# Performance work log

Hardware: AMD Instinct MI355X
Metric: run time of the kernel (lower is better)

## Reference

```python
import jax, jax.numpy as jnp
import numpy as np
import math

N_LAYERS = 8
D = 1024
H = 16
DK = D // H
T = 1024
V = 32000
B = 2
DFF = 4 * D
EPS = 1e-5


def layernorm(x, scale, bias):
    mu = jnp.mean(x, axis=-1, keepdims=True)
    var = jnp.mean(jnp.square(x - mu), axis=-1, keepdims=True)
    return (x - mu) * jax.lax.rsqrt(var + EPS) * scale + bias


def setup_inputs() -> dict:
    key = jax.random.key(0)
    ks = jax.random.split(key, 32)
    s = 0.02
    rn = lambda k, shape: jax.random.normal(k, shape, dtype=jnp.float32) * s
    x = jax.random.randint(ks[0], (B, T), 0, V)
    return {
        "x": x,
        "inp_emb": rn(ks[1], (V, D)),
        "pos_emb": rn(ks[2], (T, D)),
        # per-layer weights stacked on leading layer axis; per-head wq/wk/wv are
        # concatenated along the output dim (mathematically identical to the
        # per-head nn.Linear list in the torch code)
        "wq": rn(ks[3], (N_LAYERS, D, D)), "bq": jnp.zeros((N_LAYERS, D), jnp.float32),
        "wk": rn(ks[4], (N_LAYERS, D, D)), "bk": jnp.zeros((N_LAYERS, D), jnp.float32),
        "wv": rn(ks[5], (N_LAYERS, D, D)), "bv": jnp.zeros((N_LAYERS, D), jnp.float32),
        "wo": rn(ks[6], (N_LAYERS, D, D)), "bo": jnp.zeros((N_LAYERS, D), jnp.float32),
        "w1": rn(ks[7], (N_LAYERS, D, DFF)), "b1": jnp.zeros((N_LAYERS, DFF), jnp.float32),
        "w2": rn(ks[8], (N_LAYERS, DFF, D)), "b2": jnp.zeros((N_LAYERS, D), jnp.float32),
        "ln1_s": jnp.ones((N_LAYERS, D), jnp.float32), "ln1_b": jnp.zeros((N_LAYERS, D), jnp.float32),
        "ln2_s": jnp.ones((N_LAYERS, D), jnp.float32), "ln2_b": jnp.zeros((N_LAYERS, D), jnp.float32),
        "lno_s": jnp.ones((D,), jnp.float32), "lno_b": jnp.zeros((D,), jnp.float32),
        "w_out": rn(ks[9], (D, V)),
    }


def reference(x, inp_emb, pos_emb, wq, bq, wk, bk, wv, bv, wo, bo,
              w1, b1, w2, b2, ln1_s, ln1_b, ln2_s, ln2_b, lno_s, lno_b, w_out):
    h = inp_emb[x] + pos_emb[jnp.arange(T)]            # [B,T,D]
    causal = jnp.tril(jnp.ones((T, T), dtype=bool))    # [T,T]
    scale = 1.0 / math.sqrt(DK)
    for i in range(N_LAYERS):
        # --- multi-head causal attention ---
        xn = layernorm(h, ln1_s[i], ln1_b[i])
        q = (xn @ wq[i] + bq[i]).reshape(B, T, H, DK)
        k = (xn @ wk[i] + bk[i]).reshape(B, T, H, DK)
        v = (xn @ wv[i] + bv[i]).reshape(B, T, H, DK)
        scores = jnp.einsum('bqhd,bkhd->bhqk', q, k) * scale
        scores = jnp.where(causal, scores, -jnp.inf)
        att = jax.nn.softmax(scores, axis=-1)           # [B,H,T,T]
        y = jnp.einsum('bhqk,bkhd->bqhd', att, v).reshape(B, T, D)
        h = h + y @ wo[i] + bo[i]
        # --- feed-forward ---
        xn = layernorm(h, ln2_s[i], ln2_b[i])
        h = h + jax.nn.gelu(xn @ w1[i] + b1[i], approximate=False) @ w2[i] + b2[i]
    h = layernorm(h, lno_s, lno_b)
    return h @ w_out                                    # logits [B,T,V]
```

## Files before the change

### kernel.cpp

```cpp
#include <hip/hip_runtime.h>
#include <cmath>

#define D_MODEL 1024
#define N_HEADS 16
#define DKH     64
#define SEQ_T   1024
#define BATCH   2
#define VOCAB   32000
#define DFF_    4096
#define NLAYERS 8

typedef __bf16 bf16x8 __attribute__((ext_vector_type(8)));
typedef __bf16 bf16x4v __attribute__((ext_vector_type(4)));
typedef float  f32x4  __attribute__((ext_vector_type(4)));

__device__ __forceinline__ float gelu_f(float x) {
    return 0.5f * x * (1.0f + erff(x * 0.70710678118654752f));
}

__device__ __forceinline__ void gload_lds16(const void* g, void* l) {
    __builtin_amdgcn_global_load_lds(
        (const __attribute__((address_space(1))) void*)g,
        (__attribute__((address_space(3))) void*)l, 16, 0, 0);
}

__global__ __launch_bounds__(256) void embed_kernel(
    const int* __restrict__ x, const float* __restrict__ inp_emb,
    const float* __restrict__ pos_emb, float* __restrict__ h)
{
    const int idx = blockIdx.x * 256 + threadIdx.x;
    const int bt  = idx >> 10;
    const int d   = idx & 1023;
    const int t   = bt & (SEQ_T - 1);
    const int tok = x[bt];
    h[idx] = inp_emb[(size_t)tok * D_MODEL + d] + pos_emb[(size_t)t * D_MODEL + d];
}

__device__ __forceinline__ void ln_row(
    const float* __restrict__ x, const float* __restrict__ sc,
    const float* __restrict__ bi, __bf16* __restrict__ o, int row, int tid)
{
    const int c = tid * 4;
    const float4 v = *(const float4*)(x + (size_t)row * D_MODEL + c);
    float sum = v.x + v.y + v.z + v.w;
    float sq  = v.x * v.x + v.y * v.y + v.z * v.z + v.w * v.w;
    #pragma unroll
    for (int off = 32; off > 0; off >>= 1) {
        sum += __shfl_xor(sum, off);
        sq  += __shfl_xor(sq, off);
    }
    __shared__ float ssum[4], ssq[4];
    const int wave = tid >> 6, lane = tid & 63;
    if (lane == 0) { ssum[wave] = sum; ssq[wave] = sq; }
    __syncthreads();
    sum = ssum[0] + ssum[1] + ssum[2] + ssum[3];
    sq  = ssq[0]  + ssq[1]  + ssq[2]  + ssq[3];
    const float mu  = sum * (1.0f / D_MODEL);
    const float var = sq * (1.0f / D_MODEL) - mu * mu;
    const float rs  = rsqrtf(var + 1e-5f);
    const float4 s4 = *(const float4*)(sc + c);
    const float4 b4 = *(const float4*)(bi + c);
    bf16x4v ov;
    ov[0] = (__bf16)((v.x - mu) * rs * s4.x + b4.x);
    ov[1] = (__bf16)((v.y - mu) * rs * s4.y + b4.y);
    ov[2] = (__bf16)((v.z - mu) * rs * s4.z + b4.z);
    ov[3] = (__bf16)((v.w - mu) * rs * s4.w + b4.w);
    *(bf16x4v*)(o + (size_t)row * D_MODEL + c) = ov;
}

__global__ __launch_bounds__(256) void layernorm_kernel(
    const float* __restrict__ x, const float* __restrict__ sc,
    const float* __restrict__ bi, __bf16* __restrict__ o)
{
    ln_row(x, sc, bi, o, blockIdx.x, threadIdx.x);
}

__global__ __launch_bounds__(256) void prep_ln_kernel(
    const float* __restrict__ h, const float* __restrict__ ln_s,
    const float* __restrict__ ln_b, __bf16* __restrict__ xn,
    const float* __restrict__ wq, const float* __restrict__ wk,
    const float* __restrict__ wv, const float* __restrict__ wo,
    const float* __restrict__ w1, const float* __restrict__ w2,
    const float* __restrict__ bq, const float* __restrict__ bk,
    const float* __restrict__ bv,
    __bf16* __restrict__ wqkvT, __bf16* __restrict__ woT,
    __bf16* __restrict__ w1T, __bf16* __restrict__ w2T,
    float* __restrict__ bqkv,
    const float* __restrict__ wout, __bf16* __restrict__ woutT)
{
    const int tid = threadIdx.x;
    const int b   = blockIdx.x;

    if (b < 2048) {
        ln_row(h, ln_s, ln_b, xn, b, tid);
        return;
    }
    const int pb = b - 2048;
    if (pb >= 12288 && pb < 12300) {
        const int j = (pb - 12288) * 256 + tid;
        bqkv[j] = (j < 1024) ? bq[j] : (j < 2048 ? bk[j - 1024] : bv[j - 2048]);
        return;
    }

    __shared__ __bf16 tile[32][36];
    const float* in;
    __bf16* out;
    int K, N, kb0, nb0;
    if (pb < 4096) {
        const int w = pb >> 10, t = pb & 1023;
        K = 1024; N = 1024; kb0 = (t >> 5) * 32; nb0 = (t & 31) * 32;
        in  = (w == 0) ? wq : (w == 1) ? wk : (w == 2) ? wv : wo;
        out = (w == 3) ? woT : wqkvT + (size_t)w * 1024 * 1024;
    } else if (pb < 8192) {
        const int t = pb - 4096;
        K = 1024; N = 4096; kb0 = (t >> 7) * 32; nb0 = (t & 127) * 32;
        in = w1; out = w1T;
    } else if (pb < 12288) {
        const int t = pb - 8192;
        K = 4096; N = 1024; kb0 = (t >> 5) * 32; nb0 = (t & 31) * 32;
        in = w2; out = w2T;
    } else {
        const int t = pb - 12300;
        K = 1024; N = VOCAB; kb0 = (t & 31) * 32; nb0 = (t >> 5) * 32;
        in = wout; out = woutT;
    }

    {
        const int rr = tid >> 3, c4 = (tid & 7) * 4;
        const float4 v = *(const float4*)(in + (size_t)(kb0 + rr) * N + nb0 + c4);
        tile[rr][c4 + 0] = (__bf16)v.x;
        tile[rr][c4 + 1] = (__bf16)v.y;
        tile[rr][c4 + 2] = (__bf16)v.z;
        tile[rr][c4 + 3] = (__bf16)v.w;
    }
    __syncthreads();
    {
        const int cc = tid >> 3, r4 = (tid & 7) * 4;
        bf16x4v ov;
        ov[0] = tile[r4 + 0][cc];
        ov[1] = tile[r4 + 1][cc];
        ov[2] = tile[r4 + 2][cc];
        ov[3] = tile[r4 + 3][cc];
        *(bf16x4v*)(out + (size_t)(nb0 + cc) * K + kb0 + r4) = ov;
    }
}

template <int BN_T, int EPI, typename OutT, bool NT = false>
__global__ __launch_bounds__(256) void gemm_bt(
    const __bf16* __restrict__ A, const __bf16* __restrict__ Bt,
    const float* __restrict__ bias, const float* __restrict__ res,
    OutT* __restrict__ C, int M, int N, int K)
{
    constexpr int NF  = BN_T / 32;
    constexpr int NCB = BN_T / 8;
    __shared__ __align__(16) char smem[(128 + BN_T) * 64 * 2];
    __bf16* As = (__bf16*)smem;
    __bf16* Bs = As + 128 * 64;

    const int tid  = threadIdx.x;
    const int wave = tid >> 6;
    const int lane = tid & 63;
    const int r    = lane & 15;
    const int kb   = lane >> 4;
    const int wm   = wave >> 1;
    const int wn   = wave & 1;

    const int ntm = gridDim.x;
    const int nwg = ntm * gridDim.y;
    int bid = blockIdx.y * ntm + blockIdx.x;
    if ((nwg & 7) == 0) bid = (bid & 7) * (nwg >> 3) + (bid >> 3);
    const int bm = (bid % ntm) * 128;
    const int bn = (bid / ntm) * BN_T;

    const int srow = lane >> 3;
    const int sg   = lane & 7;

    f32x4 acc[4][NF] = {};

    for (int k0 = 0; k0 < K; k0 += 64) {
        #pragma unroll
        for (int i = 0; i < 4; ++i) {
            const int c    = i * 4 + wave;
            const int row  = c * 8 + srow;
            const int scol = (sg ^ (row & 7)) * 8;
            gload_lds16(A + (size_t)(bm + row) * K + k0 + scol, &As[c * 512]);
        }
        #pragma unroll
        for (int i = 0; i < NCB / 4; ++i) {
            const int c    = i * 4 + wave;
            const int row  = c * 8 + srow;
            const int scol = (sg ^ (row & 7)) * 8;
            gload_lds16(Bt + (size_t)(bn + row) * K + k0 + scol, &Bs[c * 512]);
        }
        __syncthreads();

        #pragma unroll
        for (int s = 0; s < 2; ++s) {
            bf16x8 af[4];
            #pragma unroll
            for (int m = 0; m < 4; ++m) {
                const int row = wm * 64 + m * 16 + r;
                const int g   = (s * 4 + kb) ^ (row & 7);
                af[m] = *(const bf16x8*)&As[row * 64 + g * 8];
            }
            #pragma unroll
            for (int n = 0; n < NF; ++n) {
                const int row = wn * (NF * 16) + n * 16 + r;
                const int g   = (s * 4 + kb) ^ (row & 7);
                const bf16x8 bfr = *(const bf16x8*)&Bs[row * 64 + g * 8];
                #pragma unroll
                for (int m = 0; m < 4; ++m)
                    acc[m][n] = __builtin_amdgcn_mfma_f32_16x16x32_bf16(af[m], bfr, acc[m][n], 0, 0, 0);
            }
        }
        __syncthreads();
    }

    if constexpr (NT) {
        float* Cs = (float*)smem;
        #pragma unroll
        for (int cchunk = 0; cchunk < 4; ++cchunk) {
            if (wm == (cchunk >> 1)) {
                #pragma unroll
                for (int mm = 0; mm < 2; ++mm) {
                    const int m = (cchunk & 1) * 2 + mm;
                    #pragma unroll
                    for (int n = 0; n < NF; ++n) {
                        const int col = wn * (NF * 16) + n * 16 + r;
                        const float bv = bias ? bias[bn + col] : 0.0f;
                        #pragma unroll
                        for (int rg = 0; rg < 4; ++rg)
                            Cs[(mm * 16 + kb * 4 + rg) * 132 + col] = acc[m][n][rg] + bv;
                    }
                }
            }
            __syncthreads();
            const int rrow = tid >> 3, g8 = tid & 7;
            const size_t grow = (size_t)(bm + cchunk * 32 + rrow) * N + bn;
            #pragma unroll
            for (int j = 0; j < 4; ++j) {
                const f32x4 v = *(const f32x4*)&Cs[rrow * 132 + j * 32 + g8 * 4];
                __builtin_nontemporal_store(v, (f32x4*)((float*)C + grow + j * 32 + g8 * 4));
            }
            __syncthreads();
        }
        return;
    }

    #pragma unroll
    for (int m = 0; m < 4; ++m) {
        const int row = bm + wm * 64 + m * 16 + kb * 4;
        #pragma unroll
        for (int n = 0; n < NF; ++n) {
            const int col = bn + wn * (NF * 16) + n * 16 + r;
            const float bv = bias ? bias[col] : 0.0f;
            #pragma unroll
            for (int rg = 0; rg < 4; ++rg) {
                float v = acc[m][n][rg] + bv;
                if constexpr (EPI == 1) v += res[(size_t)(row + rg) * N + col];
                if constexpr (EPI == 2) v = gelu_f(v);
                C[(size_t)(row + rg) * N + col] = (OutT)v;
            }
        }
    }
}

struct AttnState {
    float m[4];
    float l[4];
    f32x4 yacc[4];
};

template <bool MASK>
__device__ __forceinline__ void attn_tile_step(
    AttnState& st, const bf16x8 (&qf)[2], int q0, int kt,
    int wave, int r, int kb,
    const __bf16 (*K_lds)[72], const __bf16 (*V_lds)[72],
    __bf16 (*P_row)[72])
{
    f32x4 sacc[4] = {};
    #pragma unroll
    for (int kc = 0; kc < 2; ++kc) {
        #pragma unroll
        for (int g = 0; g < 4; ++g) {
            const bf16x8 kf = *(const bf16x8*)&K_lds[g * 16 + r][kc * 32 + kb * 8];
            sacc[g] = __builtin_amdgcn_mfma_f32_16x16x32_bf16(qf[kc], kf, sacc[g], 0, 0, 0);
        }
    }

    float s[4][4], p[4][4];
    #pragma unroll
    for (int g = 0; g < 4; ++g) {
        #pragma unroll
        for (int rg = 0; rg < 4; ++rg) {
            if constexpr (MASK) {
                const int key = kt * 64 + g * 16 + r;
                const int qq  = q0 + wave * 16 + kb * 4 + rg;
                s[g][rg] = (key <= qq) ? sacc[g][rg] * 0.125f : -INFINITY;
            } else {
                s[g][rg] = sacc[g][rg] * 0.125f;
            }
        }
    }

    float mt[4];
    #pragma unroll
    for (int rg = 0; rg < 4; ++rg)
        mt[rg] = fmaxf(fmaxf(s[0][rg], s[1][rg]), fmaxf(s[2][rg], s[3][rg]));
    #pragma unroll
    for (int off = 1; off < 16; off <<= 1) {
        #pragma unroll
        for (int rg = 0; rg < 4; ++rg) mt[rg] = fmaxf(mt[rg], __shfl_xor(mt[rg], off));
    }

    bool grow = false;
    #pragma unroll
    for (int rg = 0; rg < 4; ++rg) grow |= (mt[rg] > st.m[rg] + 8.0f);
    if (__any(grow)) {
        #pragma unroll
        for (int rg = 0; rg < 4; ++rg) {
            const float mn   = fmaxf(st.m[rg], mt[rg]);
            const float corr = __expf(st.m[rg] - mn);
            st.l[rg] *= corr;
            st.m[rg]  = mn;
            #pragma unroll
            for (int n = 0; n < 4; ++n) st.yacc[n][rg] *= corr;
        }
    }

    float psum[4];
    #pragma unroll
    for (int rg = 0; rg < 4; ++rg) {
        psum[rg] = 0.0f;
        #pragma unroll
        for (int g = 0; g < 4; ++g) {
            p[g][rg] = __expf(s[g][rg] - st.m[rg]);
            psum[rg] += p[g][rg];
        }
    }
    #pragma unroll
    for (int off = 1; off < 16; off <<= 1) {
        #pragma unroll
        for (int rg = 0; rg < 4; ++rg) psum[rg] += __shfl_xor(psum[rg], off);
    }
    #pragma unroll
    for (int rg = 0; rg < 4; ++rg) st.l[rg] += psum[rg];

    #pragma unroll
    for (int g = 0; g < 4; ++g) {
        #pragma unroll
        for (int rg = 0; rg < 4; ++rg)
            P_row[kb * 4 + rg][g * 16 + r] = (__bf16)p[g][rg];
    }
    const bf16x8 pa0 = *(const bf16x8*)&P_row[r][kb * 8];
    const bf16x8 pa1 = *(const bf16x8*)&P_row[r][32 + kb * 8];

    #pragma unroll
    for (int n = 0; n < 4; ++n) {
        const int vrow = n * 16 + r;
        const int swz  = (vrow >> 3) & 7;
        const bf16x8 vf0 = *(const bf16x8*)&V_lds[vrow][(kb ^ swz) * 8];
        st.yacc[n] = __builtin_amdgcn_mfma_f32_16x16x32_bf16(pa0, vf0, st.yacc[n], 0, 0, 0);
    }
    #pragma unroll
    for (int n = 0; n < 4; ++n) {
        const int vrow = n * 16 + r;
        const int swz  = (vrow >> 3) & 7;
        const bf16x8 vf1 = *(const bf16x8*)&V_lds[vrow][((kb + 4) ^ swz) * 8];
        st.yacc[n] = __builtin_amdgcn_mfma_f32_16x16x32_bf16(pa1, vf1, st.yacc[n], 0, 0, 0);
    }
}

__global__ __launch_bounds__(256) void attn_mfma_kernel(
    const __bf16* __restrict__ qkv, __bf16* __restrict__ y)
{
    constexpr int QS = 3 * D_MODEL;
    __shared__ __align__(16) __bf16 K_lds[64][72];
    __shared__ __align__(16) __bf16 V_lds[64][72];
    __shared__ __align__(16) __bf16 P_lds[4][16][72];

    const int tid  = threadIdx.x;
    const int wave = tid >> 6;
    const int lane = tid & 63;
    const int r    = lane & 15;
    const int kb   = lane >> 4;

    const int ip  = blockIdx.x;
    const int q0A = ip * 64;
    const int q0B = (15 - ip) * 64;
    const int b   = blockIdx.y >> 4;
    const int h   = blockIdx.y & 15;

    const __bf16* qp = qkv + (size_t)b * SEQ_T * QS + h * DKH;
    const __bf16* kp = qp + D_MODEL;
    const __bf16* vp = qp + 2 * D_MODEL;
    __bf16* yp = y + (size_t)b * SEQ_T * D_MODEL + h * DKH;

    bf16x8 qfA[2], qfB[2];
    {
        const int qrA = q0A + wave * 16 + r;
        const int qrB = q0B + wave * 16 + r;
        #pragma unroll
        for (int kc = 0; kc < 2; ++kc) {
            qfA[kc] = *(const bf16x8*)(qp + (size_t)qrA * QS + kc * 32 + kb * 8);
            qfB[kc] = *(const bf16x8*)(qp + (size_t)qrB * QS + kc * 32 + kb * 8);
        }
    }

    AttnState stA, stB;
    #pragma unroll
    for (int rg = 0; rg < 4; ++rg) {
        stA.m[rg] = -INFINITY; stA.l[rg] = 0.0f;
        stB.m[rg] = -INFINITY; stB.l[rg] = 0.0f;
    }
    #pragma unroll
    for (int n = 0; n < 4; ++n) { stA.yacc[n] = {}; stB.yacc[n] = {}; }

    const int skey = tid >> 2;
    const int sg16 = (tid & 3) * 16;
    const int swz0 = ((sg16 >> 3) & 7) * 8;
    const int swz1 = (((sg16 + 8) >> 3) & 7) * 8;

    const int ntiles = 16 - ip;

    bf16x8 kr0, kr1, vr0, vr1;
    {
        const size_t go = (size_t)skey * QS;
        kr0 = *(const bf16x8*)(kp + go + sg16);
        kr1 = *(const bf16x8*)(kp + go + sg16 + 8);
        vr0 = *(const bf16x8*)(vp + go + sg16);
        vr1 = *(const bf16x8*)(vp + go + sg16 + 8);
    }

    for (int kt = 0; kt < ntiles; ++kt) {
        *(bf16x8*)&K_lds[skey][sg16]     = kr0;
        *(bf16x8*)&K_lds[skey][sg16 + 8] = kr1;
        #pragma unroll
        for (int j = 0; j < 8; ++j)
            V_lds[sg16 + j][skey ^ swz0] = vr0[j];
        #pragma unroll
        for (int j = 0; j < 8; ++j)
            V_lds[sg16 + 8 + j][skey ^ swz1] = vr1[j];
        __syncthreads();

        if (kt + 1 < ntiles) {
            const size_t go = (size_t)((kt + 1) * 64 + skey) * QS;
            kr0 = *(const bf16x8*)(kp + go + sg16);
            kr1 = *(const bf16x8*)(kp + go + sg16 + 8);
            vr0 = *(const bf16x8*)(vp + go + sg16);
            vr1 = *(const bf16x8*)(vp + go + sg16 + 8);
        }

        if (kt == ntiles - 1)
            attn_tile_step<true >(stB, qfB, q0B, kt, wave, r, kb, K_lds, V_lds, P_lds[wave]);
        else
            attn_tile_step<false>(stB, qfB, q0B, kt, wave, r, kb, K_lds, V_lds, P_lds[wave]);
        if (kt <= ip) {
            if (kt == ip)
                attn_tile_step<true >(stA, qfA, q0A, kt, wave, r, kb, K_lds, V_lds, P_lds[wave]);
            else
                attn_tile_step<false>(stA, qfA, q0A, kt, wave, r, kb, K_lds, V_lds, P_lds[wave]);
        }
        __syncthreads();
    }

    float invA[4], invB[4];
    #pragma unroll
    for (int rg = 0; rg < 4; ++rg) {
        invA[rg] = 1.0f / stA.l[rg];
        invB[rg] = 1.0f / stB.l[rg];
    }
    #pragma unroll
    for (int n = 0; n < 4; ++n) {
        #pragma unroll
        for (int rg = 0; rg < 4; ++rg) {
            const int rowA = q0A + wave * 16 + kb * 4 + rg;
            const int rowB = q0B + wave * 16 + kb * 4 + rg;
            yp[(size_t)rowA * D_MODEL + n * 16 + r] = (__bf16)(stA.yacc[n][rg] * invA[rg]);
            yp[(size_t)rowB * D_MODEL + n * 16 + r] = (__bf16)(stB.yacc[n][rg] * invB[rg]);
        }
    }
}

extern "C" void kernel_launch(void* const* d_in, const int* in_sizes, int n_in,
                              void* d_out, int out_size, void* d_ws, size_t ws_size,
                              hipStream_t stream)
{
    const int*   x       = (const int*)  d_in[0];
    const float* inp_emb = (const float*)d_in[1];
    const float* pos_emb = (const float*)d_in[2];
    const float* wq = (const float*)d_in[3];
    const float* bq = (const float*)d_in[4];
    const float* wk = (const float*)d_in[5];
    const float* bk = (const float*)d_in[6];
    const float* wv = (const float*)d_in[7];
    const float* bv = (const float*)d_in[8];
    const float* wo = (const float*)d_in[9];
    const float* bo = (const float*)d_in[10];
    const float* w1 = (const float*)d_in[11];
    const float* b1 = (const float*)d_in[12];
    const float* w2 = (const float*)d_in[13];
    const float* b2 = (const float*)d_in[14];
    const float* ln1_s = (const float*)d_in[15];
    const float* ln1_b = (const float*)d_in[16];
    const float* ln2_s = (const float*)d_in[17];
    const float* ln2_b = (const float*)d_in[18];
    const float* lno_s = (const float*)d_in[19];
    const float* lno_b = (const float*)d_in[20];
    const float* w_out = (const float*)d_in[21];

    const int M = BATCH * SEQ_T;
    const size_t MB = 1u << 20;

    char* w = (char*)d_ws;
    float*  h     = (float*) (w + 0);
    __bf16* xn    = (__bf16*)(w + 8  * MB);
    __bf16* yb    = (__bf16*)(w + 12 * MB);
    __bf16* sh    = (__bf16*)(w + 16 * MB);
    __bf16* wqkvT = (__bf16*)(w + 32 * MB);
    __bf16* woT   = (__bf16*)(w + 38 * MB);
    __bf16* w1T   = (__bf16*)(w + 40 * MB);
    __bf16* w2T   = (__bf16*)(w + 48 * MB);
    float*  bqkv  = (float*) (w + 56 * MB);
    __bf16* woutT = (__bf16*)(w + 57 * MB);

    embed_kernel<<<dim3(M * D_MODEL / 256), 256, 0, stream>>>(x, inp_emb, pos_emb, h);

    for (int i = 0; i < NLAYERS; ++i) {
        const size_t wOff  = (size_t)i * D_MODEL * D_MODEL;
        const size_t w1Off = (size_t)i * D_MODEL * DFF_;

        const int nblk = 2048 + 12300 + (i == 0 ? 32000 : 0);
        prep_ln_kernel<<<dim3(nblk), 256, 0, stream>>>(
            h, ln1_s + i * D_MODEL, ln1_b + i * D_MODEL, xn,
            wq + wOff, wk + wOff, wv + wOff, wo + wOff, w1 + w1Off, w2 + w1Off,
            bq + i * D_MODEL, bk + i * D_MODEL, bv + i * D_MODEL,
            wqkvT, woT, w1T, w2T, bqkv,
            (i == 0) ? w_out : nullptr, woutT);

        gemm_bt<64, 0, __bf16><<<dim3(M / 128, 3 * D_MODEL / 64), 256, 0, stream>>>(
            xn, wqkvT, bqkv, nullptr, sh, M, 3 * D_MODEL, D_MODEL);
        attn_mfma_kernel<<<dim3(8, BATCH * N_HEADS), 256, 0, stream>>>(sh, yb);
        gemm_bt<64, 1, float><<<dim3(M / 128, D_MODEL / 64), 256, 0, stream>>>(
            yb, woT, bo + i * D_MODEL, h, h, M, D_MODEL, D_MODEL);
        layernorm_kernel<<<dim3(M), 256, 0, stream>>>(h, ln2_s + i * D_MODEL, ln2_b + i * D_MODEL, xn);
        gemm_bt<128, 2, __bf16><<<dim3(M / 128, DFF_ / 128), 256, 0, stream>>>(
            xn, w1T, b1 + i * DFF_, nullptr, sh, M, DFF_, D_MODEL);
        gemm_bt<64, 1, float><<<dim3(M / 128, D_MODEL / 64), 256, 0, stream>>>(
            sh, w2T, b2 + i * D_MODEL, h, h, M, D_MODEL, DFF_);
    }

    layernorm_kernel<<<dim3(M), 256, 0, stream>>>(h, lno_s, lno_b, xn);
    gemm_bt<128, 0, float, true><<<dim3(M / 128, VOCAB / 128), 256, 0, stream>>>(
        xn, woutT, nullptr, nullptr, (float*)d_out, M, VOCAB, D_MODEL);
}
```

Baseline: 1.661 ms.

## Widen weight transpose tiles to 32x64 and simplify nontemporal GEMM epilogue

The fused LN/weight-transpose kernel now handles 32x64 tiles per block, so each thread loads two float4s and writes a 16-byte bf16x8 vector. This halves the block count and makes the transposed stores wider. The GEMM drops its LDS-staged, coalesced nontemporal epilogue for the output projection and writes directly with per-element nontemporal stores, with shared memory split into separate A/B arrays. The epilogue change gives up coalesced 16-byte logits writes in favor of scattered scalar stores, which may hurt the large vocab GEMM.

Measured after the change: 1.697 ms. +2.2%, slower.

```diff
diff --git a/kernel.cpp b/kernel.cpp
--- a/kernel.cpp
+++ b/kernel.cpp
@@ -96,52 +96,56 @@
         return;
     }
     const int pb = b - 2048;
-    if (pb >= 12288 && pb < 12300) {
-        const int j = (pb - 12288) * 256 + tid;
+    if (pb >= 6144 && pb < 6156) {
+        const int j = (pb - 6144) * 256 + tid;
         bqkv[j] = (j < 1024) ? bq[j] : (j < 2048 ? bk[j - 1024] : bv[j - 2048]);
         return;
     }
 
-    __shared__ __bf16 tile[32][36];
+    __shared__ __bf16 tile[32][72];
     const float* in;
     __bf16* out;
     int K, N, kb0, nb0;
-    if (pb < 4096) {
-        const int w = pb >> 10, t = pb & 1023;
-        K = 1024; N = 1024; kb0 = (t >> 5) * 32; nb0 = (t & 31) * 32;
+    if (pb < 2048) {
+        const int w = pb >> 9, t = pb & 511;
+        K = 1024; N = 1024; kb0 = (t >> 4) * 32; nb0 = (t & 15) * 64;
         in  = (w == 0) ? wq : (w == 1) ? wk : (w == 2) ? wv : wo;
         out = (w == 3) ? woT : wqkvT + (size_t)w * 1024 * 1024;
-    } else if (pb < 8192) {
+    } else if (pb < 4096) {
+        const int t = pb - 2048;
+        K = 1024; N = 4096; kb0 = (t >> 6) * 32; nb0 = (t & 63) * 64;
+        in = w1; out = w1T;
+    } else if (pb < 6144) {
         const int t = pb - 4096;
-        K = 1024; N = 4096; kb0 = (t >> 7) * 32; nb0 = (t & 127) * 32;
-        in = w1; out = w1T;
-    } else if (pb < 12288) {
-        const int t = pb - 8192;
-        K = 4096; N = 1024; kb0 = (t >> 5) * 32; nb0 = (t & 31) * 32;
+        K = 4096; N = 1024; kb0 = (t >> 4) * 32; nb0 = (t & 15) * 64;
         in = w2; out = w2T;
     } else {
-        const int t = pb - 12300;
-        K = 1024; N = VOCAB; kb0 = (t & 31) * 32; nb0 = (t >> 5) * 32;
+        const int t = pb - 6156;
+        K = 1024; N = VOCAB; kb0 = (t & 31) * 32; nb0 = (t >> 5) * 64;
         in = wout; out = woutT;
     }
 
     {
-        const int rr = tid >> 3, c4 = (tid & 7) * 4;
-        const float4 v = *(const float4*)(in + (size_t)(kb0 + rr) * N + nb0 + c4);
-        tile[rr][c4 + 0] = (__bf16)v.x;
-        tile[rr][c4 + 1] = (__bf16)v.y;
-        tile[rr][c4 + 2] = (__bf16)v.z;
-        tile[rr][c4 + 3] = (__bf16)v.w;
+        const int rr = tid >> 3, c8 = (tid & 7) * 8;
+        const float* p = in + (size_t)(kb0 + rr) * N + nb0 + c8;
+        const float4 v0 = *(const float4*)p;
+        const float4 v1 = *(const float4*)(p + 4);
+        tile[rr][c8 + 0] = (__bf16)v0.x;
+        tile[rr][c8 + 1] = (__bf16)v0.y;
+        tile[rr][c8 + 2] = (__bf16)v0.z;
+        tile[rr][c8 + 3] = (__bf16)v0.w;
+        tile[rr][c8 + 4] = (__bf16)v1.x;
+        tile[rr][c8 + 5] = (__bf16)v1.y;
+        tile[rr][c8 + 6] = (__bf16)v1.z;
+        tile[rr][c8 + 7] = (__bf16)v1.w;
     }
     __syncthreads();
     {
-        const int cc = tid >> 3, r4 = (tid & 7) * 4;
-        bf16x4v ov;
-        ov[0] = tile[r4 + 0][cc];
-        ov[1] = tile[r4 + 1][cc];
-        ov[2] = tile[r4 + 2][cc];
-        ov[3] = tile[r4 + 3][cc];
-        *(bf16x4v*)(out + (size_t)(nb0 + cc) * K + kb0 + r4) = ov;
+        const int cc = tid >> 2, k8 = (tid & 3) * 8;
+        bf16x8 ov;
+        #pragma unroll
+        for (int e = 0; e < 8; ++e) ov[e] = tile[k8 + e][cc];
+        *(bf16x8*)(out + (size_t)(nb0 + cc) * K + kb0 + k8) = ov;
     }
 }
 
@@ -153,9 +157,8 @@
 {
     constexpr int NF  = BN_T / 32;
     constexpr int NCB = BN_T / 8;
-    __shared__ __align__(16) char smem[(128 + BN_T) * 64 * 2];
-    __bf16* As = (__bf16*)smem;
-    __bf16* Bs = As + 128 * 64;
+    __shared__ __bf16 As[128 * 64];
+    __shared__ __bf16 Bs[BN_T * 64];
 
     const int tid  = threadIdx.x;
     const int wave = tid >> 6;
@@ -216,37 +219,6 @@
         __syncthreads();
     }
 
-    if constexpr (NT) {
-        float* Cs = (float*)smem;
-        #pragma unroll
-        for (int cchunk = 0; cchunk < 4; ++cchunk) {
-            if (wm == (cchunk >> 1)) {
-                #pragma unroll
-                for (int mm = 0; mm < 2; ++mm) {
-                    const int m = (cchunk & 1) * 2 + mm;
-                    #pragma unroll
-                    for (int n = 0; n < NF; ++n) {
-                        const int col = wn * (NF * 16) + n * 16 + r;
-                        const float bv = bias ? bias[bn + col] : 0.0f;
-                        #pragma unroll
-                        for (int rg = 0; rg < 4; ++rg)
-                            Cs[(mm * 16 + kb * 4 + rg) * 132 + col] = acc[m][n][rg] + bv;
-                    }
-                }
-            }
-            __syncthreads();
-            const int rrow = tid >> 3, g8 = tid & 7;
-            const size_t grow = (size_t)(bm + cchunk * 32 + rrow) * N + bn;
-            #pragma unroll
-            for (int j = 0; j < 4; ++j) {
-                const f32x4 v = *(const f32x4*)&Cs[rrow * 132 + j * 32 + g8 * 4];
-                __builtin_nontemporal_store(v, (f32x4*)((float*)C + grow + j * 32 + g8 * 4));
-            }
-            __syncthreads();
-        }
-        return;
-    }
-
     #pragma unroll
     for (int m = 0; m < 4; ++m) {
         const int row = bm + wm * 64 + m * 16 + kb * 4;
@@ -259,7 +231,11 @@
                 float v = acc[m][n][rg] + bv;
                 if constexpr (EPI == 1) v += res[(size_t)(row + rg) * N + col];
                 if constexpr (EPI == 2) v = gelu_f(v);
-                C[(size_t)(row + rg) * N + col] = (OutT)v;
+                if constexpr (NT) {
+                    __builtin_nontemporal_store((OutT)v, &C[(size_t)(row + rg) * N + col]);
+                } else {
+                    C[(size_t)(row + rg) * N + col] = (OutT)v;
+                }
             }
         }
     }
@@ -530,7 +506,7 @@
         const size_t wOff  = (size_t)i * D_MODEL * D_MODEL;
         const size_t w1Off = (size_t)i * D_MODEL * DFF_;
 
-        const int nblk = 2048 + 12300 + (i == 0 ? 32000 : 0);
+        const int nblk = 2048 + 6156 + (i == 0 ? 16000 : 0);
         prep_ln_kernel<<<dim3(nblk), 256, 0, stream>>>(
             h, ln1_s + i * D_MODEL, ln1_b + i * D_MODEL, xn,
             wq + wOff, wk + wOff, wv + wOff, wo + wOff, w1 + w1Off, w2 + w1Off,
```
